# Performance work log

Hardware: AMD Instinct MI355X
Metric: run time of the kernel (lower is better)

Reference implementation:

```python
import jax, jax.numpy as jnp
import numpy as np

B, C, H, W = 16, 256, 32, 32
DIM = H * W  # LayerNorm/Linear dim == h*w per the rearrange in forward


def _conv1x1(x, w, b):
    # x: [b,c,h,w], w: [out,in] (1x1 kernel squeezed), b: [out]
    return jnp.einsum('bchw,oc->bohw', x, w) + b[None, :, None, None]


def _layernorm(x, g, b, eps=1e-5):
    mu = jnp.mean(x, axis=-1, keepdims=True)
    var = jnp.var(x, axis=-1, keepdims=True)
    return (x - mu) / jnp.sqrt(var + eps) * g + b


def setup_inputs() -> dict:
    key = jax.random.key(0)
    ks = jax.random.split(key, 12)
    n = jax.random.normal
    k_cdc = (2.0 / (2 * C)) ** 0.5   # kaiming_normal fan_in = 2C
    k_v = (2.0 / C) ** 0.5           # fan_in = C
    k_lin = (2.0 / DIM) ** 0.5       # fan_in = DIM
    return {
        'x_spa': n(ks[0], (B, C, H, W), jnp.float32),
        'x_freq': n(ks[1], (B, C, H, W), jnp.float32),
        'w_cdc': n(ks[2], (C, 2 * C), jnp.float32) * k_cdc,
        'b_cdc': jnp.zeros((C,), jnp.float32),
        'w_sv': n(ks[3], (C, C), jnp.float32) * k_v,
        'b_sv': jnp.zeros((C,), jnp.float32),
        'w_fv': n(ks[4], (C, C), jnp.float32) * k_v,
        'b_fv': jnp.zeros((C,), jnp.float32),
        'ln_w': jnp.ones((DIM,), jnp.float32),
        'ln_b': jnp.zeros((DIM,), jnp.float32),
        'w_qk': n(ks[5], (2 * DIM, DIM), jnp.float32) * k_lin,  # Linear(dim, 2*dim), no bias
        'w_spa': n(ks[6], (DIM, DIM), jnp.float32) * k_lin,
        'b_spa': jnp.zeros((DIM,), jnp.float32),
        'w_frq': n(ks[7], (DIM, DIM), jnp.float32) * k_lin,
        'b_frq': jnp.zeros((DIM,), jnp.float32),
    }


def reference(x_spa, x_freq, w_cdc, b_cdc, w_sv, b_sv, w_fv, b_fv,
              ln_w, ln_b, w_qk, w_spa, b_spa, w_frq, b_frq):
    b, c, h, w = x_spa.shape
    hw = h * w
    scale = hw ** (-0.5)
    v_spa = _conv1x1(x_spa, w_sv, b_sv).reshape(b, c, hw)
    v_freq = _conv1x1(x_freq, w_fv, b_fv).reshape(b, c, hw)
    x = _conv1x1(jnp.concatenate([x_spa, x_freq], axis=1), w_cdc, b_cdc).reshape(b, c, hw)
    x = _layernorm(x, ln_w, ln_b)
    qk = x @ w_qk.T                       # [b, c, 2*hw]
    q, k = jnp.split(qk, 2, axis=-1)      # each [b, c, hw]
    att = jnp.einsum('bcn,bcm->bnm', q, k) * scale   # q^T k over channels: [b, hw, hw]
    att_spa = jax.nn.softmax(att @ w_spa.T + b_spa, axis=-1)
    att_frq = jax.nn.softmax(att @ w_frq.T + b_frq, axis=-1)
    out_spa = x_spa + jnp.einsum('bcn,bnm->bcm', v_spa, att_spa).reshape(b, c, h, w)
    out_freq = x_freq + jnp.einsum('bcn,bnm->bcm', v_freq, att_frq).reshape(b, c, h, w)
    return out_spa, out_freq
```

## Files before the change

kernel.cpp:

```cpp
#include <hip/hip_runtime.h>
#include <hip/hip_bf16.h>

typedef __hip_bfloat16 bf16;
typedef __attribute__((ext_vector_type(8))) short bf16x8v;
typedef __attribute__((ext_vector_type(4))) float f32x4v;

__device__ __forceinline__ float bfbits2f(unsigned short h) {
    union { unsigned int u; float f; } v; v.u = ((unsigned int)h) << 16; return v.f;
}
__device__ __forceinline__ unsigned short f2bfbits(float f) {
    bf16 h = __float2bfloat16(f);
    unsigned short s;
    __builtin_memcpy(&s, &h, 2);
    return s;
}
__device__ __forceinline__ float load1_any(const void* p, long idx, bool f32) {
    if (f32) return ((const float*)p)[idx];
    return bfbits2f(((const unsigned short*)p)[idx]);
}
__device__ __forceinline__ float4 loadbf4(const bf16* p) {
    ushort4 u = *reinterpret_cast<const ushort4*>(p);
    return make_float4(bfbits2f(u.x), bfbits2f(u.y), bfbits2f(u.z), bfbits2f(u.w));
}
__device__ __forceinline__ void store_bf4(bf16* p, float a, float b, float c, float d) {
    ushort4 o;
    o.x = f2bfbits(a); o.y = f2bfbits(b); o.z = f2bfbits(c); o.w = f2bfbits(d);
    *reinterpret_cast<ushort4*>(p) = o;
}
__device__ __forceinline__ void gl16(const void* g, void* l) {
    __builtin_amdgcn_global_load_lds(
        (const __attribute__((address_space(1))) unsigned int*)g,
        (__attribute__((address_space(3))) unsigned int*)l, 16, 0, 0);
}

__global__ __launch_bounds__(1024)
void detect_kernel(const unsigned short* __restrict__ x, int* __restrict__ flag) {
    const int tid = threadIdx.x;
    int zc = 0, hc = 0;
    const uint4* xv = (const uint4*)x;
#pragma unroll
    for (int p = 0; p < 16; ++p) {
        uint4 v = xv[p * 1024 + tid];
        unsigned s0 = v.x & 0xFFFFu, s1 = v.y & 0xFFFFu;
        unsigned s2 = v.z & 0xFFFFu, s3 = v.w & 0xFFFFu;
        zc += (int)(s0 == 0) + (int)(s1 == 0) + (int)(s2 == 0) + (int)(s3 == 0);
        hc += (int)(((s0 >> 7) & 0xFFu) >= 0x90u) + (int)(((s1 >> 7) & 0xFFu) >= 0x90u)
            + (int)(((s2 >> 7) & 0xFFu) >= 0x90u) + (int)(((s3 >> 7) & 0xFFu) >= 0x90u);
    }
#pragma unroll
    for (int off = 32; off > 0; off >>= 1) {
        zc += __shfl_down(zc, off);
        hc += __shfl_down(hc, off);
    }
    __shared__ int rz[16], rh[16];
    if ((tid & 63) == 0) { rz[tid >> 6] = zc; rh[tid >> 6] = hc; }
    __syncthreads();
    if (tid == 0) {
        int Z = 0, H = 0;
#pragma unroll
        for (int i = 0; i < 16; ++i) { Z += rz[i]; H += rh[i]; }
        *flag = (Z > 60000 || H > 256) ? 1 : 0;
    }
}

__global__ void diag_kernel(float* __restrict__ out, float val) {
    if (threadIdx.x == 0) out[0] = val;
}

__global__ __launch_bounds__(256)
void convert6_kernel(const void* __restrict__ s0, const void* __restrict__ s1,
                     const void* __restrict__ s2, const void* __restrict__ s3,
                     const void* __restrict__ s4, const void* __restrict__ s5,
                     bf16* __restrict__ dst, const int* __restrict__ dflag) {
    const bool f32 = (*dflag != 0);
    for (long i = (long)blockIdx.x * 256 + threadIdx.x; i < 4456448;
         i += (long)gridDim.x * 256) {
        const void* s; long o;
        if (i < 131072)       { s = s0; o = i; }
        else if (i < 196608)  { s = s1; o = i - 131072; }
        else if (i < 262144)  { s = s2; o = i - 196608; }
        else if (i < 2359296) { s = s3; o = i - 262144; }
        else if (i < 3407872) { s = s4; o = i - 2359296; }
        else                  { s = s5; o = i - 3407872; }
        dst[i] = __float2bfloat16(load1_any(s, o, f32));
    }
}

__global__ __launch_bounds__(256)
void xpose_conv_kernel(const void* __restrict__ x1, const void* __restrict__ x2,
                       bf16* __restrict__ dst, int bofs, int zsplit,
                       const int* __restrict__ dflag) {
    const bool f32 = (*dflag != 0);
    __shared__ float t[64][65];
    const int ch0 = blockIdx.y * 64, n0 = blockIdx.x * 64, z = blockIdx.z;
    const bool hiz = (z >= zsplit);
    const int zl = hiz ? z - zsplit : z;
    const void* x = hiz ? x2 : x1;
    const long sb = (long)(zl + bofs) * 262144, db = (long)z * 262144;
    const int tid = threadIdx.x;
#pragma unroll
    for (int p = 0; p < 16; ++p) {
        int e = tid + p * 256; int sch = e >> 6, sn = e & 63;
        t[sch][sn] = load1_any(x, sb + (long)(ch0 + sch) * 1024 + n0 + sn, f32);
    }
    __syncthreads();
#pragma unroll
    for (int p = 0; p < 16; ++p) {
        int e = tid + p * 256; int dn = e >> 6, dch = e & 63;
        dst[db + (long)(n0 + dn) * 256 + ch0 + dch] = __float2bfloat16(t[dch][dn]);
    }
}

__global__ __launch_bounds__(256)
void sm_stats_kernel(const bf16* __restrict__ x, float2* __restrict__ st) {
    const int tid = threadIdx.x, lane = tid & 63, w = tid >> 6;
    const long row = (long)blockIdx.x * 4 + w;
    const bf16* p = x + row * 1024;
    float4 v[4];
    float m = -3.4e38f;
#pragma unroll
    for (int c = 0; c < 4; ++c) {
        v[c] = loadbf4(p + lane * 4 + c * 256);
        m = fmaxf(m, fmaxf(fmaxf(v[c].x, v[c].y), fmaxf(v[c].z, v[c].w)));
    }
#pragma unroll
    for (int off = 32; off > 0; off >>= 1) m = fmaxf(m, __shfl_xor(m, off));
    float s = 0.f;
#pragma unroll
    for (int c = 0; c < 4; ++c)
        s += __expf(v[c].x - m) + __expf(v[c].y - m) + __expf(v[c].z - m) + __expf(v[c].w - m);
#pragma unroll
    for (int off = 32; off > 0; off >>= 1) s += __shfl_xor(s, off);
    if (lane == 0) st[row] = make_float2(m, 1.0f / s);
}

__global__ __launch_bounds__(256)
void xpose_norm_kernel(const bf16* __restrict__ src, bf16* __restrict__ dst,
                       const float2* __restrict__ st) {
    __shared__ float t[64][65];
    const int c0 = blockIdx.x * 64, r0 = blockIdx.y * 64;
    const long b = (long)blockIdx.z * 1048576;
    const long sb = (long)blockIdx.z * 1024;
    const int tid = threadIdx.x;
#pragma unroll
    for (int p = 0; p < 16; ++p) {
        int e = tid + p * 256; int r = e >> 6, c = e & 63;
        float2 ms = st[sb + r0 + r];
        t[r][c] = __expf(__bfloat162float(src[b + (long)(r0 + r) * 1024 + c0 + c]) - ms.x) * ms.y;
    }
    __syncthreads();
#pragma unroll
    for (int p = 0; p < 16; ++p) {
        int e = tid + p * 256; int r = e >> 6, c = e & 63;
        dst[b + (long)(c0 + r) * 1024 + r0 + c] = __float2bfloat16(t[c][r]);
    }
}

template <int EPI>
__global__ __launch_bounds__(256)
void mfma_nt(const bf16* __restrict__ A1, const bf16* __restrict__ A2,
             long aBatch, int ldA,
             const bf16* __restrict__ B1, const bf16* __restrict__ B2,
             long bBatch, int ldB, int ksplit, long kOff2,
             void* __restrict__ out1, void* __restrict__ out2,
             long oBatch, int ldO, int K, float scale,
             const void* __restrict__ bias1, const void* __restrict__ bias2,
             const void* __restrict__ res1, const void* __restrict__ res2,
             long rBatch, int bofs, int zsplit,
             const int* __restrict__ dflag) {
    __shared__ short As[3][4096];
    __shared__ short Bs[3][4096];
    const int tid  = threadIdx.x;
    const int lane = tid & 63, wave = tid >> 6;
    const int quad = lane >> 4, lrow = lane & 15;
    const int wm = (wave >> 1) * 64, wn = (wave & 1) * 64;
    const int n0 = blockIdx.x * 128, m0 = blockIdx.y * 128;
    const int z  = blockIdx.z;
    const bool hiz = (z >= zsplit);
    const int zl = hiz ? z - zsplit : z;
    const int srow = tid >> 2, sseg = tid & 3;
    const int sl = sseg ^ ((srow >> 1) & 3);
    const int xq = quad ^ ((lrow >> 1) & 3);

    const bf16* Ab = (hiz ? A2 : A1) + (long)zl * aBatch;
    const bf16* Bb = (hiz ? B2 : B1) + (long)zl * bBatch;

    auto stage = [&](int buf, int k0) {
        const bf16* asrc = Ab + (long)k0;
        const bf16* bsrc = Bb + ((k0 < ksplit) ? (long)k0 : (long)(k0 - ksplit) + kOff2);
        const bf16* ga0 = asrc + (long)(m0 + srow) * ldA + sl * 8;
        const bf16* ga1 = asrc + (long)(m0 + 64 + srow) * ldA + sl * 8;
        const bf16* gb0 = bsrc + (long)(n0 + srow) * ldB + sl * 8;
        const bf16* gb1 = bsrc + (long)(n0 + 64 + srow) * ldB + sl * 8;
        short* la = &As[buf][wave * 512];
        short* lb = &Bs[buf][wave * 512];
        gl16(ga0, la);
        gl16(ga1, la + 2048);
        gl16(gb0, lb);
        gl16(gb1, lb + 2048);
    };

    f32x4v acc[4][4] = {};
    const int nt = K >> 5;
    stage(0, 0);
    if (nt > 1) stage(1, 32);
    if (nt > 2) stage(2, 64);

    int cur = 0;
    for (int t = 0; t < nt; ++t) {
        const int rem = nt - 1 - t;
        if (rem >= 2)      asm volatile("s_waitcnt vmcnt(8)" ::: "memory");
        else if (rem == 1) asm volatile("s_waitcnt vmcnt(4)" ::: "memory");
        else               asm volatile("s_waitcnt vmcnt(0)" ::: "memory");
        __builtin_amdgcn_s_barrier();
        __builtin_amdgcn_sched_barrier(0);
        bf16x8v bfr[4], afr[4];
#pragma unroll
        for (int j = 0; j < 4; ++j)
            bfr[j] = *(const bf16x8v*)&Bs[cur][(wn + j * 16 + lrow) * 32 + xq * 8];
#pragma unroll
        for (int i = 0; i < 4; ++i)
            afr[i] = *(const bf16x8v*)&As[cur][(wm + i * 16 + lrow) * 32 + xq * 8];
        asm volatile("s_waitcnt lgkmcnt(0)" ::: "memory");
        __builtin_amdgcn_sched_barrier(0);
        __builtin_amdgcn_s_barrier();
        __builtin_amdgcn_sched_barrier(0);
        if (t + 3 < nt) stage(cur, (t + 3) << 5);
#pragma unroll
        for (int i = 0; i < 4; ++i)
#pragma unroll
            for (int j = 0; j < 4; ++j)
                acc[i][j] = __builtin_amdgcn_mfma_f32_16x16x32_bf16(afr[i], bfr[j], acc[i][j], 0, 0, 0);
        cur = (cur == 2) ? 0 : cur + 1;
    }

    const bool f32 = (*dflag != 0);
    const void* bias = hiz ? bias2 : bias1;
    if (EPI <= 2) {
        bf16* O = (bf16*)(hiz ? out2 : out1) + (long)zl * oBatch;
#pragma unroll
        for (int i = 0; i < 4; ++i) {
            int row0 = m0 + wm + i * 16 + quad * 4;
            float rb[4] = {0.f, 0.f, 0.f, 0.f};
            if (EPI == 1) {
#pragma unroll
                for (int r = 0; r < 4; ++r) rb[r] = load1_any(bias, row0 + r, f32);
            }
#pragma unroll
            for (int j = 0; j < 4; ++j) {
                int col = n0 + wn + j * 16 + lrow;
                float cb = (EPI == 2) ? load1_any(bias, col, f32) : 0.f;
#pragma unroll
                for (int r = 0; r < 4; ++r) {
                    float vv = acc[i][j][r];
                    if (EPI == 1) vv += rb[r];
                    if (EPI == 2) vv = vv * scale + cb;
                    O[(long)(row0 + r) * ldO + col] = __float2bfloat16(vv);
                }
            }
        }
    } else {
        float* O = (float*)(hiz ? out2 : out1);
        const void* res = hiz ? res2 : res1;
        const long ob  = (long)(zl + bofs) * oBatch;
        const long rbb = (long)(zl + bofs) * rBatch;
#pragma unroll
        for (int i = 0; i < 4; ++i) {
            int row0 = m0 + wm + i * 16 + quad * 4;
#pragma unroll
            for (int j = 0; j < 4; ++j) {
                int col = n0 + wn + j * 16 + lrow;
#pragma unroll
                for (int r = 0; r < 4; ++r) {
                    float rv = load1_any(res, rbb + (long)(row0 + r) * ldO + col, f32);
                    O[ob + (long)(row0 + r) * ldO + col] = acc[i][j][r] + rv;
                }
            }
        }
    }
}

__global__ __launch_bounds__(256)
void layernorm_kernel(bf16* __restrict__ x, const void* __restrict__ g,
                      const void* __restrict__ beta, const int* __restrict__ dflag) {
    const bool f32 = (*dflag != 0);
    bf16* p = x + (long)blockIdx.x * 1024;
    const int tid = threadIdx.x;
    float4 v = loadbf4(p + tid * 4);
    float s  = v.x + v.y + v.z + v.w;
    float ss = v.x * v.x + v.y * v.y + v.z * v.z + v.w * v.w;
#pragma unroll
    for (int off = 32; off > 0; off >>= 1) {
        s  += __shfl_down(s, off);
        ss += __shfl_down(ss, off);
    }
    __shared__ float sh[8];
    __shared__ float sh_mu, sh_rs;
    if ((tid & 63) == 0) { sh[tid >> 6] = s; sh[4 + (tid >> 6)] = ss; }
    __syncthreads();
    if (tid == 0) {
        float S  = sh[0] + sh[1] + sh[2] + sh[3];
        float SS = sh[4] + sh[5] + sh[6] + sh[7];
        float mu = S * (1.0f / 1024.0f);
        float var = SS * (1.0f / 1024.0f) - mu * mu;
        sh_mu = mu;
        sh_rs = rsqrtf(fmaxf(var, 0.0f) + 1e-5f);
    }
    __syncthreads();
    float mu = sh_mu, rs = sh_rs;
    float gx = load1_any(g, tid * 4 + 0, f32), gy = load1_any(g, tid * 4 + 1, f32);
    float gz = load1_any(g, tid * 4 + 2, f32), gw = load1_any(g, tid * 4 + 3, f32);
    float bx = load1_any(beta, tid * 4 + 0, f32), by = load1_any(beta, tid * 4 + 1, f32);
    float bz = load1_any(beta, tid * 4 + 2, f32), bw = load1_any(beta, tid * 4 + 3, f32);
    store_bf4(p + tid * 4,
              (v.x - mu) * rs * gx + bx, (v.y - mu) * rs * gy + by,
              (v.z - mu) * rs * gz + bz, (v.w - mu) * rs * gw + bw);
}

extern "C" void kernel_launch(void* const* d_in, const int* in_sizes, int n_in,
                              void* d_out, int out_size, void* d_ws, size_t ws_size,
                              hipStream_t stream) {
    const void* x_spa  = d_in[0];
    const void* x_freq = d_in[1];
    const void* w_cdc  = d_in[2];
    const void* b_cdc  = d_in[3];
    const void* w_sv   = d_in[4];
    const void* b_sv   = d_in[5];
    const void* w_fv   = d_in[6];
    const void* b_fv   = d_in[7];
    const void* ln_w   = d_in[8];
    const void* ln_b   = d_in[9];
    const void* w_qk   = d_in[10];
    const void* w_spa  = d_in[11];
    const void* b_spa  = d_in[12];
    const void* w_frq  = d_in[13];
    const void* b_frq  = d_in[14];
    float* out = (float*)d_out;

    const int B = 16, C = 256;
    const long XB = 262144;
    const long PB = 1048576;

    int*  dflag = (int*)d_ws;
    bf16* wb    = (bf16*)((char*)d_ws + 4096);
    bf16* w_cdc_b = wb;
    bf16* w_sv_b  = w_cdc_b + 131072;
    bf16* w_fv_b  = w_sv_b  + 65536;
    bf16* w_qk_b  = w_fv_b  + 65536;
    bf16* w_spa_b = w_qk_b  + 2097152;
    bf16* w_frq_b = w_spa_b + 1048576;
    bf16* pb      = w_frq_b + 1048576;

    const size_t fixedB = 4096 + 4456448ull * 2;
    const size_t perB   = 13123584ull;
    size_t avail = (ws_size > fixedB) ? (ws_size - fixedB) : 0;
    long gmax = (long)(avail / perB);
    const bool wsOK = (gmax >= 1);
    int G = wsOK ? (int)(gmax > 16 ? 16 : gmax) : 1;

    bf16* xT   = pb;
    bf16* xln  = xT   + 2L * G * XB;
    bf16* kb   = xln  + (long)G * XB;
    bf16* qT   = kb   + (long)G * XB;
    bf16* TT   = qT   + (long)G * XB;
    bf16* vb   = TT   + 2L * G * XB;
    bf16* attp = vb   + 2L * G * XB;
    bf16* attpT= attp + 2L * G * PB;
    float2* stats = (float2*)(attpT + 2L * G * PB);

    dim3 blk(256);
    detect_kernel<<<dim3(1), dim3(1024), 0, stream>>>((const unsigned short*)x_spa, dflag);

    if (!wsOK) {
        float mb = (float)(ws_size >> 20);
        diag_kernel<<<dim3(1), dim3(64), 0, stream>>>(out, 1000.0f * (mb + 1.0f));
        return;
    }

    convert6_kernel<<<dim3(4352), blk, 0, stream>>>(w_cdc, w_sv, w_fv, w_qk, w_spa, w_frq,
                                                    wb, dflag);

    for (int b0 = 0; b0 < B; b0 += G) {
        int g = (B - b0 < G) ? (B - b0) : G;

        xpose_conv_kernel<<<dim3(16, 4, 2 * g), blk, 0, stream>>>(
            x_spa, x_freq, xT, b0, g, dflag);

        mfma_nt<1><<<dim3(8, 2, 2 * g), blk, 0, stream>>>(
            w_sv_b, w_fv_b, 0, 256,
            xT, xT + (long)g * XB, XB, 256, 256, 0,
            vb, vb + (long)g * XB, XB, 1024, 256, 1.0f,
            b_sv, b_fv, nullptr, nullptr, 0, 0, g, dflag);

        mfma_nt<1><<<dim3(8, 2, g), blk, 0, stream>>>(
            w_cdc_b, w_cdc_b, 0, 512,
            xT, xT, XB, 256, 256, (long)g * XB,
            xln, xln, XB, 1024, 512, 1.0f,
            b_cdc, b_cdc, nullptr, nullptr, 0, 0, g, dflag);
        layernorm_kernel<<<dim3(g * C), blk, 0, stream>>>(xln, ln_w, ln_b, dflag);

        mfma_nt<0><<<dim3(8, 2, g), blk, 0, stream>>>(
            xln, xln, XB, 1024,
            w_qk_b + 1048576, w_qk_b + 1048576, 0, 1024, 1024, 0,
            kb, kb, XB, 1024, 1024, 1.0f,
            nullptr, nullptr, nullptr, nullptr, 0, 0, g, dflag);
        mfma_nt<0><<<dim3(2, 8, g), blk, 0, stream>>>(
            w_qk_b, w_qk_b, 0, 1024,
            xln, xln, XB, 1024, 1024, 0,
            qT, qT, XB, 256, 1024, 1.0f,
            nullptr, nullptr, nullptr, nullptr, 0, 0, g, dflag);

        mfma_nt<0><<<dim3(2, 8, 2 * g), blk, 0, stream>>>(
            w_spa_b, w_frq_b, 0, 1024,
            kb, kb, XB, 1024, 1024, 0,
            TT, TT + (long)g * XB, XB, 256, 1024, 1.0f,
            nullptr, nullptr, nullptr, nullptr, 0, 0, g, dflag);

        mfma_nt<2><<<dim3(8, 8, 2 * g), blk, 0, stream>>>(
            qT, qT, XB, 256,
            TT, TT + (long)g * XB, XB, 256, 256, 0,
            attp, attp + (long)g * PB, PB, 1024, 256, 0.03125f,
            b_spa, b_frq, nullptr, nullptr, 0, 0, g, dflag);

        sm_stats_kernel<<<dim3(512 * g), blk, 0, stream>>>(attp, stats);
        xpose_norm_kernel<<<dim3(16, 16, 2 * g), blk, 0, stream>>>(attp, attpT, stats);

        mfma_nt<3><<<dim3(8, 2, 2 * g), blk, 0, stream>>>(
            vb, vb + (long)g * XB, XB, 1024,
            attpT, attpT + (long)g * PB, PB, 1024, 1024, 0,
            out, out + 4194304, XB, 1024, 1024, 1.0f,
            nullptr, nullptr, x_spa, x_freq, XB, b0, g, dflag);
    }
}
```

Baseline: 371.5 us.

## Compute transposed attention directly, fold softmax normalization into V projection, deepen pipeline

The attention GEMM now swaps its operands so it writes the transposed score matrix directly, which removes the separate stats and transpose-normalize passes. A new column-wise kernel exponentiates the scores in place and records inverse sums. Those inverse sums are applied as a per-column scale in the V projection epilogue, which now runs after the softmax. The K and Q projections are merged into one launch using per-half strides and a grid-swap flag. The GEMM staging ring grows from 3 to 5 LDS buffers with 4 stages in flight. The trade-offs are more shared memory per block, which may lower occupancy, and strided column reads in the softmax kernel, which may coalesce poorly.

```diff
diff --git a/kernel.cpp b/kernel.cpp
--- a/kernel.cpp
+++ b/kernel.cpp
@@ -112,78 +112,73 @@
 }
 
 __global__ __launch_bounds__(256)
-void sm_stats_kernel(const bf16* __restrict__ x, float2* __restrict__ st) {
-    const int tid = threadIdx.x, lane = tid & 63, w = tid >> 6;
-    const long row = (long)blockIdx.x * 4 + w;
-    const bf16* p = x + row * 1024;
-    float4 v[4];
+void smnorm_kernel(bf16* __restrict__ X, float* __restrict__ invS) {
+    const int tid = threadIdx.x, c = tid & 63, jp = tid >> 6;
+    const int n0 = blockIdx.x * 64;
+    const long zb = (long)blockIdx.y * 1048576;
+    bf16* Xp = X + zb + n0 + c;
     float m = -3.4e38f;
-#pragma unroll
-    for (int c = 0; c < 4; ++c) {
-        v[c] = loadbf4(p + lane * 4 + c * 256);
-        m = fmaxf(m, fmaxf(fmaxf(v[c].x, v[c].y), fmaxf(v[c].z, v[c].w)));
-    }
-#pragma unroll
-    for (int off = 32; off > 0; off >>= 1) m = fmaxf(m, __shfl_xor(m, off));
+#pragma unroll 4
+    for (int it = 0; it < 256; ++it) {
+        float v = bfbits2f(((const unsigned short*)Xp)[(long)(jp * 256 + it) * 1024]);
+        m = fmaxf(m, v);
+    }
+    __shared__ float sh[4][64];
+    sh[jp][c] = m;
+    __syncthreads();
+    const float M = fmaxf(fmaxf(sh[0][c], sh[1][c]), fmaxf(sh[2][c], sh[3][c]));
+    __syncthreads();
     float s = 0.f;
-#pragma unroll
-    for (int c = 0; c < 4; ++c)
-        s += __expf(v[c].x - m) + __expf(v[c].y - m) + __expf(v[c].z - m) + __expf(v[c].w - m);
-#pragma unroll
-    for (int off = 32; off > 0; off >>= 1) s += __shfl_xor(s, off);
-    if (lane == 0) st[row] = make_float2(m, 1.0f / s);
-}
-
-__global__ __launch_bounds__(256)
-void xpose_norm_kernel(const bf16* __restrict__ src, bf16* __restrict__ dst,
-                       const float2* __restrict__ st) {
-    __shared__ float t[64][65];
-    const int c0 = blockIdx.x * 64, r0 = blockIdx.y * 64;
-    const long b = (long)blockIdx.z * 1048576;
-    const long sb = (long)blockIdx.z * 1024;
-    const int tid = threadIdx.x;
-#pragma unroll
-    for (int p = 0; p < 16; ++p) {
-        int e = tid + p * 256; int r = e >> 6, c = e & 63;
-        float2 ms = st[sb + r0 + r];
-        t[r][c] = __expf(__bfloat162float(src[b + (long)(r0 + r) * 1024 + c0 + c]) - ms.x) * ms.y;
-    }
-    __syncthreads();
-#pragma unroll
-    for (int p = 0; p < 16; ++p) {
-        int e = tid + p * 256; int r = e >> 6, c = e & 63;
-        dst[b + (long)(c0 + r) * 1024 + r0 + c] = __float2bfloat16(t[c][r]);
-    }
+#pragma unroll 4
+    for (int it = 0; it < 256; ++it) {
+        long off = (long)(jp * 256 + it) * 1024;
+        float v = bfbits2f(((const unsigned short*)Xp)[off]);
+        float e = __expf(v - M);
+        ((unsigned short*)Xp)[off] = f2bfbits(e);
+        s += e;
+    }
+    __syncthreads();
+    sh[jp][c] = s;
+    __syncthreads();
+    if (jp == 0)
+        invS[(long)blockIdx.y * 1024 + n0 + c] =
+            1.0f / (sh[0][c] + sh[1][c] + sh[2][c] + sh[3][c]);
 }
 
 template <int EPI>
 __global__ __launch_bounds__(256)
 void mfma_nt(const bf16* __restrict__ A1, const bf16* __restrict__ A2,
-             long aBatch, int ldA,
+             long aB1, long aB2, int ldA1, int ldA2,
              const bf16* __restrict__ B1, const bf16* __restrict__ B2,
-             long bBatch, int ldB, int ksplit, long kOff2,
+             long bB1, long bB2, int ldB1, int ldB2,
+             int ksplit, long kOff2,
              void* __restrict__ out1, void* __restrict__ out2,
-             long oBatch, int ldO, int K, float scale,
+             long oB1, long oB2, int ldO1, int ldO2,
+             int K, float scale,
              const void* __restrict__ bias1, const void* __restrict__ bias2,
              const void* __restrict__ res1, const void* __restrict__ res2,
-             long rBatch, int bofs, int zsplit,
+             long rBatch, int bofs, int zsplit, int swapXY,
              const int* __restrict__ dflag) {
-    __shared__ short As[3][4096];
-    __shared__ short Bs[3][4096];
+    __shared__ short As[5][4096];
+    __shared__ short Bs[5][4096];
     const int tid  = threadIdx.x;
     const int lane = tid & 63, wave = tid >> 6;
     const int quad = lane >> 4, lrow = lane & 15;
     const int wm = (wave >> 1) * 64, wn = (wave & 1) * 64;
-    const int n0 = blockIdx.x * 128, m0 = blockIdx.y * 128;
     const int z  = blockIdx.z;
     const bool hiz = (z >= zsplit);
     const int zl = hiz ? z - zsplit : z;
+    const bool sw = hiz && swapXY;
+    const int n0 = (sw ? blockIdx.y : blockIdx.x) * 128;
+    const int m0 = (sw ? blockIdx.x : blockIdx.y) * 128;
+    const int ldA = hiz ? ldA2 : ldA1, ldB = hiz ? ldB2 : ldB1;
+    const int ldO = hiz ? ldO2 : ldO1;
     const int srow = tid >> 2, sseg = tid & 3;
     const int sl = sseg ^ ((srow >> 1) & 3);
     const int xq = quad ^ ((lrow >> 1) & 3);
 
-    const bf16* Ab = (hiz ? A2 : A1) + (long)zl * aBatch;
-    const bf16* Bb = (hiz ? B2 : B1) + (long)zl * bBatch;
+    const bf16* Ab = (hiz ? A2 : A1) + (long)zl * (hiz ? aB2 : aB1);
+    const bf16* Bb = (hiz ? B2 : B1) + (long)zl * (hiz ? bB2 : bB1);
 
     auto stage = [&](int buf, int k0) {
         const bf16* asrc = Ab + (long)k0;
@@ -205,11 +200,13 @@
     stage(0, 0);
     if (nt > 1) stage(1, 32);
     if (nt > 2) stage(2, 64);
+    if (nt > 3) stage(3, 96);
 
     int cur = 0;
     for (int t = 0; t < nt; ++t) {
         const int rem = nt - 1 - t;
-        if (rem >= 2)      asm volatile("s_waitcnt vmcnt(8)" ::: "memory");
+        if (rem >= 3)      asm volatile("s_waitcnt vmcnt(12)" ::: "memory");
+        else if (rem == 2) asm volatile("s_waitcnt vmcnt(8)" ::: "memory");
         else if (rem == 1) asm volatile("s_waitcnt vmcnt(4)" ::: "memory");
         else               asm volatile("s_waitcnt vmcnt(0)" ::: "memory");
         __builtin_amdgcn_s_barrier();
@@ -225,36 +222,42 @@
         __builtin_amdgcn_sched_barrier(0);
         __builtin_amdgcn_s_barrier();
         __builtin_amdgcn_sched_barrier(0);
-        if (t + 3 < nt) stage(cur, (t + 3) << 5);
+        if (t + 4 < nt) {
+            int nb = cur + 4; if (nb >= 5) nb -= 5;
+            stage(nb, (t + 4) << 5);
+        }
 #pragma unroll
         for (int i = 0; i < 4; ++i)
 #pragma unroll
             for (int j = 0; j < 4; ++j)
                 acc[i][j] = __builtin_amdgcn_mfma_f32_16x16x32_bf16(afr[i], bfr[j], acc[i][j], 0, 0, 0);
-        cur = (cur == 2) ? 0 : cur + 1;
+        cur = (cur == 4) ? 0 : cur + 1;
     }
 
     const bool f32 = (*dflag != 0);
     const void* bias = hiz ? bias2 : bias1;
-    if (EPI <= 2) {
-        bf16* O = (bf16*)(hiz ? out2 : out1) + (long)zl * oBatch;
+    if (EPI != 3) {
+        bf16* O = (bf16*)(hiz ? out2 : out1) + (long)zl * (hiz ? oB2 : oB1);
+        const float* csp = (EPI == 4)
+            ? (const float*)(hiz ? res2 : res1) + (long)zl * rBatch : nullptr;
 #pragma unroll
         for (int i = 0; i < 4; ++i) {
             int row0 = m0 + wm + i * 16 + quad * 4;
             float rb[4] = {0.f, 0.f, 0.f, 0.f};
-            if (EPI == 1) {
+            if (EPI == 1 || EPI == 2 || EPI == 4) {
 #pragma unroll
                 for (int r = 0; r < 4; ++r) rb[r] = load1_any(bias, row0 + r, f32);
             }
 #pragma unroll
             for (int j = 0; j < 4; ++j) {
                 int col = n0 + wn + j * 16 + lrow;
-                float cb = (EPI == 2) ? load1_any(bias, col, f32) : 0.f;
+                float cs = (EPI == 4) ? csp[col] : 1.0f;
 #pragma unroll
                 for (int r = 0; r < 4; ++r) {
                     float vv = acc[i][j][r];
                     if (EPI == 1) vv += rb[r];
-                    if (EPI == 2) vv = vv * scale + cb;
+                    if (EPI == 2) vv = vv * scale + rb[r];
+                    if (EPI == 4) vv = (vv + rb[r]) * cs;
                     O[(long)(row0 + r) * ldO + col] = __float2bfloat16(vv);
                 }
             }
@@ -262,7 +265,7 @@
     } else {
         float* O = (float*)(hiz ? out2 : out1);
         const void* res = hiz ? res2 : res1;
-        const long ob  = (long)(zl + bofs) * oBatch;
+        const long ob  = (long)(zl + bofs) * (hiz ? oB2 : oB1);
         const long rbb = (long)(zl + bofs) * rBatch;
 #pragma unroll
         for (int i = 0; i < 4; ++i) {
@@ -352,21 +355,20 @@
     bf16* pb      = w_frq_b + 1048576;
 
     const size_t fixedB = 4096 + 4456448ull * 2;
-    const size_t perB   = 13123584ull;
+    const size_t perB   = 8921088ull;
     size_t avail = (ws_size > fixedB) ? (ws_size - fixedB) : 0;
     long gmax = (long)(avail / perB);
     const bool wsOK = (gmax >= 1);
     int G = wsOK ? (int)(gmax > 16 ? 16 : gmax) : 1;
 
-    bf16* xT   = pb;
-    bf16* xln  = xT   + 2L * G * XB;
-    bf16* kb   = xln  + (long)G * XB;
-    bf16* qT   = kb   + (long)G * XB;
-    bf16* TT   = qT   + (long)G * XB;
-    bf16* vb   = TT   + 2L * G * XB;
-    bf16* attp = vb   + 2L * G * XB;
-    bf16* attpT= attp + 2L * G * PB;
-    float2* stats = (float2*)(attpT + 2L * G * PB);
+    bf16* xT    = pb;
+    bf16* xln   = xT   + 2L * G * XB;
+    bf16* kb    = xln  + (long)G * XB;
+    bf16* qT    = kb   + (long)G * XB;
+    bf16* TT    = qT   + (long)G * XB;
+    bf16* vb    = TT   + 2L * G * XB;
+    bf16* attpT = vb   + 2L * G * XB;
+    float* invS = (float*)(attpT + 2L * G * PB);
 
     dim3 blk(256);
     detect_kernel<<<dim3(1), dim3(1024), 0, stream>>>((const unsigned short*)x_spa, dflag);
@@ -386,49 +388,43 @@
         xpose_conv_kernel<<<dim3(16, 4, 2 * g), blk, 0, stream>>>(
             x_spa, x_freq, xT, b0, g, dflag);
 
-        mfma_nt<1><<<dim3(8, 2, 2 * g), blk, 0, stream>>>(
-            w_sv_b, w_fv_b, 0, 256,
-            xT, xT + (long)g * XB, XB, 256, 256, 0,
-            vb, vb + (long)g * XB, XB, 1024, 256, 1.0f,
-            b_sv, b_fv, nullptr, nullptr, 0, 0, g, dflag);
-
         mfma_nt<1><<<dim3(8, 2, g), blk, 0, stream>>>(
-            w_cdc_b, w_cdc_b, 0, 512,
-            xT, xT, XB, 256, 256, (long)g * XB,
-            xln, xln, XB, 1024, 512, 1.0f,
-            b_cdc, b_cdc, nullptr, nullptr, 0, 0, g, dflag);
+            w_cdc_b, w_cdc_b, 0, 0, 512, 512,
+            xT, xT, XB, XB, 256, 256, 256, (long)g * XB,
+            xln, xln, XB, XB, 1024, 1024,
+            512, 1.0f, b_cdc, b_cdc, nullptr, nullptr, 0, 0, g, 0, dflag);
         layernorm_kernel<<<dim3(g * C), blk, 0, stream>>>(xln, ln_w, ln_b, dflag);
 
-        mfma_nt<0><<<dim3(8, 2, g), blk, 0, stream>>>(
-            xln, xln, XB, 1024,
-            w_qk_b + 1048576, w_qk_b + 1048576, 0, 1024, 1024, 0,
-            kb, kb, XB, 1024, 1024, 1.0f,
-            nullptr, nullptr, nullptr, nullptr, 0, 0, g, dflag);
-        mfma_nt<0><<<dim3(2, 8, g), blk, 0, stream>>>(
-            w_qk_b, w_qk_b, 0, 1024,
-            xln, xln, XB, 1024, 1024, 0,
-            qT, qT, XB, 256, 1024, 1.0f,
-            nullptr, nullptr, nullptr, nullptr, 0, 0, g, dflag);
+        mfma_nt<0><<<dim3(8, 2, 2 * g), blk, 0, stream>>>(
+            xln, w_qk_b, XB, 0, 1024, 1024,
+            w_qk_b + 1048576, xln, 0, XB, 1024, 1024, 1024, 0,
+            kb, qT, XB, XB, 1024, 256,
+            1024, 1.0f, nullptr, nullptr, nullptr, nullptr, 0, 0, g, 1, dflag);
 
         mfma_nt<0><<<dim3(2, 8, 2 * g), blk, 0, stream>>>(
-            w_spa_b, w_frq_b, 0, 1024,
-            kb, kb, XB, 1024, 1024, 0,
-            TT, TT + (long)g * XB, XB, 256, 1024, 1.0f,
-            nullptr, nullptr, nullptr, nullptr, 0, 0, g, dflag);
+            w_spa_b, w_frq_b, 0, 0, 1024, 1024,
+            kb, kb, XB, XB, 1024, 1024, 1024, 0,
+            TT, TT + (long)g * XB, XB, XB, 256, 256,
+            1024, 1.0f, nullptr, nullptr, nullptr, nullptr, 0, 0, g, 0, dflag);
 
         mfma_nt<2><<<dim3(8, 8, 2 * g), blk, 0, stream>>>(
-            qT, qT, XB, 256,
-            TT, TT + (long)g * XB, XB, 256, 256, 0,
-            attp, attp + (long)g * PB, PB, 1024, 256, 0.03125f,
-            b_spa, b_frq, nullptr, nullptr, 0, 0, g, dflag);
-
-        sm_stats_kernel<<<dim3(512 * g), blk, 0, stream>>>(attp, stats);
-        xpose_norm_kernel<<<dim3(16, 16, 2 * g), blk, 0, stream>>>(attp, attpT, stats);
+            TT, TT + (long)g * XB, XB, XB, 256, 256,
+            qT, qT, XB, XB, 256, 256, 256, 0,
+            attpT, attpT + (long)g * PB, PB, PB, 1024, 1024,
+            256, 0.03125f, b_spa, b_frq, nullptr, nullptr, 0, 0, g, 0, dflag);
+
+        smnorm_kernel<<<dim3(16, 2 * g), blk, 0, stream>>>(attpT, invS);
+
+        mfma_nt<4><<<dim3(8, 2, 2 * g), blk, 0, stream>>>(
+            w_sv_b, w_fv_b, 0, 0, 256, 256,
+            xT, xT + (long)g * XB, XB, XB, 256, 256, 256, 0,
+            vb, vb + (long)g * XB, XB, XB, 1024, 1024,
+            256, 1.0f, b_sv, b_fv, invS, invS + (long)g * 1024, 1024, 0, g, 0, dflag);
 
         mfma_nt<3><<<dim3(8, 2, 2 * g), blk, 0, stream>>>(
-            vb, vb + (long)g * XB, XB, 1024,
-            attpT, attpT + (long)g * PB, PB, 1024, 1024, 0,
-            out, out + 4194304, XB, 1024, 1024, 1.0f,
-            nullptr, nullptr, x_spa, x_freq, XB, b0, g, dflag);
-    }
-}
+            vb, vb + (long)g * XB, XB, XB, 1024, 1024,
+            attpT, attpT + (long)g * PB, PB, PB, 1024, 1024, 1024, 0,
+            out, out + 4194304, XB, XB, 1024, 1024,
+            1024, 1.0f, nullptr, nullptr, x_spa, x_freq, XB, b0, g, 0, dflag);
+    }
+}
```

After: 396.8 us. +6.8%, slower.
